# Performance work log

Hardware: AMD Instinct MI355X
Metric: run time of the kernel (lower is better)

## Reference

```python
import jax, jax.numpy as jnp
import numpy as np

B = 2048          # query batch
DIM = 256         # embedding dim (first component timelike)
SLOTS = 65536     # memory slots, count N == SLOTS (full memory)
K_TOP = 32
SIM_THRESHOLD = 0.0
LOOP_EPS = 1e-3
DECAY = 0.99


def setup_inputs() -> dict:
    key = jax.random.key(0)
    k1, k2, k3 = jax.random.split(key, 3)
    q = jax.random.normal(k1, (B, DIM), dtype=jnp.float32)
    mem = jax.random.normal(k2, (SLOTS, DIM), dtype=jnp.float32)
    age = jax.random.uniform(k3, (SLOTS,), dtype=jnp.float32) * 50.0
    return {"q": q, "mem": mem, "age": age}


def _eigen_similarity(q, mem):
    # Lorentz-invariant (Minkowski) similarity, normalized to [-1, 1].
    # metric = diag(+1, -1, ..., -1): first component timelike.
    d = q.shape[-1]
    metric = jnp.concatenate([jnp.ones((1,), q.dtype), -jnp.ones((d - 1,), q.dtype)])
    inner = jnp.einsum('bd,nd->bn', q * metric, mem)              # (B, N)
    qn = jnp.sqrt(jnp.abs(jnp.sum(q * q * metric, axis=-1))) + 1e-6   # (B,)
    mn = jnp.sqrt(jnp.abs(jnp.sum(mem * mem * metric, axis=-1))) + 1e-6  # (N,)
    return jnp.clip(inner / (qn[:, None] * mn[None, :]), -1.0, 1.0)


def reference(q, mem, age):
    sim = _eigen_similarity(q, mem)                               # (B, N)
    # loop prevention: |sim| < eps treated as self/lightlike -> zeroed
    sim = jnp.where(jnp.abs(sim) < LOOP_EPS, jnp.zeros_like(sim), sim)
    # threshold mask: disconnected entries -> -inf
    sim = jnp.where(sim <= SIM_THRESHOLD, -jnp.inf, sim)
    # temporal decay as additive log-bias
    decay_factor = jnp.clip(DECAY ** age, 1e-6, None)             # (N,)
    sim = sim + jnp.log(decay_factor)[None, :]
    sim_topk, idx_topk = jax.lax.top_k(sim, K_TOP)                # (B, k) each
    attn = jax.nn.softmax(sim_topk, axis=-1)                      # (B, k)
    mem_topk = mem[idx_topk]                                      # (B, k, D) gather
    retrieved = jnp.einsum('bk,bkd->bd', attn, mem_topk)          # (B, D)
    return retrieved
```

## Files before the change

kernel.cpp:

```cpp
#include <hip/hip_runtime.h>
#include <hip/hip_bf16.h>
#include <math.h>

#define BQ 2048
#define DIM 256
#define SLOTS 65536
#define KTOP 32
#define CAP 256
#define LCAP 10
#define POOL 48
#define TAU0 0.11f

typedef __attribute__((ext_vector_type(8))) short short8;
typedef __attribute__((ext_vector_type(4))) float f32x4;
typedef unsigned long long u64;

__device__ inline unsigned mono(float f) {
    unsigned u = __float_as_uint(f);
    return u ^ ((0u - (u >> 31)) | 0x80000000u);
}

__device__ inline ushort f2bf(float x) {
    __hip_bfloat16 h = __float2bfloat16(x);
    return *(ushort*)&h;
}

__device__ __forceinline__ void gl2lds16(const void* g, void* l) {
    __builtin_amdgcn_global_load_lds((__attribute__((address_space(1))) void*)(void*)g,
                                     (__attribute__((address_space(3))) void*)l, 16, 0, 0);
}

__global__ __launch_bounds__(256) void prep_mem_k(
    const float* __restrict__ mem, const float* __restrict__ age,
    ushort* __restrict__ mhat, float* __restrict__ mn, float* __restrict__ logdec,
    unsigned* __restrict__ counts)
{
    int t = threadIdx.x, lane = t & 63, w = t >> 6;
    if (blockIdx.x < BQ / 256) counts[blockIdx.x * 256 + t] = 0u;
    int slot = blockIdx.x * 4 + w;
    const float4* row = (const float4*)(mem + (size_t)slot * DIM);
    float4 v = row[lane];
    float p = -(v.x*v.x + v.y*v.y + v.z*v.z + v.w*v.w);
    if (lane == 0) p += 2.f * v.x * v.x;
    for (int m = 1; m < 64; m <<= 1) p += __shfl_xor(p, m);
    float nv = sqrtf(fabsf(p)) + 1e-6f;
    if (lane == 0) {
        mn[slot] = nv;
        float df = powf(0.99f, age[slot]);
        if (df < 1e-6f) df = 1e-6f;
        logdec[slot] = logf(df);
    }
    float inv = 1.f / nv;
    ushort4 o;
    o.x = f2bf(v.x * inv); o.y = f2bf(v.y * inv);
    o.z = f2bf(v.z * inv); o.w = f2bf(v.w * inv);
    *(ushort4*)&mhat[(size_t)slot * DIM + lane * 4] = o;
}

__global__ __launch_bounds__(256) void prep_q_k(
    const float* __restrict__ q, ushort* __restrict__ qhat, float* __restrict__ qs)
{
    int t = threadIdx.x, lane = t & 63, w = t >> 6;
    int b = blockIdx.x * 4 + w;
    const float4* row = (const float4*)(q + (size_t)b * DIM);
    float4 v = row[lane];
    float p = -(v.x*v.x + v.y*v.y + v.z*v.z + v.w*v.w);
    if (lane == 0) p += 2.f * v.x * v.x;
    for (int m = 1; m < 64; m <<= 1) p += __shfl_xor(p, m);
    float nv = sqrtf(fabsf(p)) + 1e-6f;
    float inv = 1.f / nv;
    float4 sv;
    sv.x = (lane == 0) ? v.x * inv : -v.x * inv;
    sv.y = -v.y * inv; sv.z = -v.z * inv; sv.w = -v.w * inv;
    *(float4*)&qs[(size_t)b * DIM + lane * 4] = sv;
    ushort4 o;
    o.x = f2bf(sv.x); o.y = f2bf(sv.y); o.z = f2bf(sv.z); o.w = f2bf(sv.w);
    *(ushort4*)&qhat[(size_t)b * DIM + lane * 4] = o;
}

__global__ __launch_bounds__(256) void screen_k(
    const ushort* __restrict__ qhat, const ushort* __restrict__ mhat,
    const float* __restrict__ logdec,
    unsigned* __restrict__ counts, u64* __restrict__ cand)
{
    __shared__ __align__(16) short At[2 * 128 * 32];
    __shared__ __align__(16) short Bt[2 * 128 * 32];
    __shared__ float tauS[128];
    __shared__ unsigned lcount[128];
    __shared__ u64 lbuf[128 * LCAP];

    int t = threadIdx.x;
    int id = blockIdx.x;
    int xcd = id & 7, slot = id >> 3;
    int rg = slot & 15, cgl = slot >> 4;
    int row0 = rg * 128;
    int col0 = (cgl * 8 + xcd) * 128;
    if (t < 128) { tauS[t] = TAU0 - logdec[col0 + t]; lcount[t] = 0u; }

    int lane = t & 63, w = t >> 6;
    int wr = (w & 1) * 64, wc = (w >> 1) * 64;
    int l15 = lane & 15, qk = (lane >> 4) * 8;
    f32x4 acc[4][4] = {};

    for (int kc = 0; kc < DIM; kc += 64) {
        __syncthreads();
        #pragma unroll
        for (int s = 0; s < 4; ++s) {
            int chunk = s * 256 + t;
            int p = chunk >> 9, rem = chunk & 511;
            int row = rem >> 2, c = rem & 3;
            char* baseA = (char*)At + s * 4096 + w * 1024;
            char* baseB = (char*)Bt + s * 4096 + w * 1024;
            gl2lds16(qhat + (size_t)(row0 + row) * DIM + kc + p * 32 + c * 8, baseA);
            gl2lds16(mhat + (size_t)(col0 + row) * DIM + kc + p * 32 + c * 8, baseB);
        }
        __syncthreads();
        #pragma unroll
        for (int p = 0; p < 2; ++p) {
            short8 af[4], bf[4];
            #pragma unroll
            for (int i = 0; i < 4; ++i)
                af[i] = *(const short8*)&At[p * 4096 + (wr + i * 16 + l15) * 32 + qk];
            #pragma unroll
            for (int i = 0; i < 4; ++i)
                bf[i] = *(const short8*)&Bt[p * 4096 + (wc + i * 16 + l15) * 32 + qk];
            #pragma unroll
            for (int i = 0; i < 4; ++i)
                #pragma unroll
                for (int j = 0; j < 4; ++j)
                    acc[i][j] = __builtin_amdgcn_mfma_f32_16x16x32_bf16(af[i], bf[j], acc[i][j], 0, 0, 0);
        }
    }

    int rquad = (lane >> 4) * 4;
    for (int i = 0; i < 4; ++i)
        for (int j = 0; j < 4; ++j) {
            int coll = wc + j * 16 + l15;
            float tau = tauS[coll];
            float ld = TAU0 - tau;
            for (int rg2 = 0; rg2 < 4; ++rg2) {
                float s = acc[i][j][rg2];
                if (s > tau) {
                    int rloc = wr + i * 16 + rquad + rg2;
                    unsigned p = atomicAdd(&lcount[rloc], 1u);
                    if (p < LCAP)
                        lbuf[rloc * LCAP + p] =
                            (((u64)mono(s + ld)) << 32) | (unsigned)(col0 + coll);
                }
            }
        }
    __syncthreads();

    if (t < 128) {
        int n = (int)lcount[t]; if (n > LCAP) n = LCAP;
        if (n > 0) {
            unsigned base = atomicAdd(&counts[row0 + t], (unsigned)n);
            for (int k = 0; k < n; ++k) {
                unsigned pos = base + (unsigned)k;
                if (pos < CAP)
                    cand[(size_t)(row0 + t) * CAP + pos] = lbuf[t * LCAP + k];
            }
        }
    }
}

__global__ __launch_bounds__(256, 4) void rescore_finalize_k(
    const float* __restrict__ qs, const float* __restrict__ mem,
    const float* __restrict__ mn, const float* __restrict__ logdec,
    const unsigned* __restrict__ counts, const u64* __restrict__ cand,
    float* __restrict__ out)
{
    __shared__ __align__(16) float qsh[DIM];
    __shared__ u64 ckey[CAP];
    __shared__ int sidx[POOL];
    __shared__ float es[POOL];
    __shared__ u64 ek[POOL];
    __shared__ float aw[KTOP];
    __shared__ int aidx[KTOP];
    __shared__ float red4a[4], red4b[4];

    int b = blockIdx.x, t = threadIdx.x;
    int lane = t & 63, wv = t >> 6;
    int cnt = (int)counts[b];
    if (cnt > CAP) cnt = CAP;
    int T = cnt < POOL ? cnt : POOL;

    qsh[t] = qs[(size_t)b * DIM + t];
    if (t < KTOP) { aw[t] = 0.f; aidx[t] = 0; }
    if (t < cnt) {
        u64 raw = cand[(size_t)b * CAP + t];
        ckey[t] = raw ^ 0xFFFFFFFFull;
    }
    __syncthreads();

    if (t < cnt) {
        u64 mykey = ckey[t];
        int rank = 0;
        for (int j = 0; j < cnt; ++j) rank += (ckey[j] > mykey);
        if (rank < POOL) sidx[rank] = (int)(~(unsigned)(mykey & 0xFFFFFFFFull));
    }
    if (t >= T && t < POOL) { es[t] = -1e30f; ek[t] = 0ull; }
    __syncthreads();

    {
        const float4* q4 = (const float4*)qsh;
        float4 qv = q4[lane];
        for (int c = wv; c < T; c += 4) {
            int si = sidx[c];
            float4 mv = ((const float4*)(mem + (size_t)si * DIM))[lane];
            float part = qv.x*mv.x + qv.y*mv.y + qv.z*mv.z + qv.w*mv.w;
            #pragma unroll
            for (int m = 1; m < 64; m <<= 1) part += __shfl_xor(part, m);
            if (lane == 0) {
                float sim = part / mn[si];
                sim = fminf(fmaxf(sim, -1.f), 1.f);
                if (fabsf(sim) < 1e-3f) sim = 0.f;
                float sc = (sim > 0.f) ? sim + logdec[si] : -1e30f;
                es[c] = sc;
                ek[c] = (((u64)mono(sc)) << 32) | (unsigned)(~(unsigned)si);
            }
        }
    }
    __syncthreads();

    float msc = -1e30f; int midx = 0; int mrank = KTOP;
    if (t < POOL) {
        u64 mykey = ek[t];
        int rank = 0;
        #pragma unroll
        for (int j = 0; j < POOL; ++j) rank += (ek[j] > mykey);
        if (rank < KTOP && es[t] > -1e29f) {
            msc = es[t];
            midx = (int)(~(unsigned)(mykey & 0xFFFFFFFFull));
            mrank = rank;
        }
    }
    float lmax = msc;
    #pragma unroll
    for (int m = 1; m < 64; m <<= 1) lmax = fmaxf(lmax, __shfl_xor(lmax, m));
    if (lane == 0) red4a[wv] = lmax;
    __syncthreads();
    float ms = fmaxf(fmaxf(red4a[0], red4a[1]), fmaxf(red4a[2], red4a[3]));

    float e = (mrank < KTOP) ? expf(msc - ms) : 0.f;
    if (mrank < KTOP) { aw[mrank] = e; aidx[mrank] = midx; }
    float ps = e;
    #pragma unroll
    for (int m = 1; m < 64; m <<= 1) ps += __shfl_xor(ps, m);
    if (lane == 0) red4b[wv] = ps;
    __syncthreads();
    float S = red4b[0] + red4b[1] + red4b[2] + red4b[3];
    float invS = (S > 0.f) ? 1.f / S : 0.f;

    float o = 0.f;
    for (int r0 = 0; r0 < KTOP; r0 += 8) {
        float w8[8]; int i8[8];
        #pragma unroll
        for (int u = 0; u < 8; ++u) { w8[u] = aw[r0 + u]; i8[u] = aidx[r0 + u]; }
        float p8[8];
        #pragma unroll
        for (int u = 0; u < 8; ++u) p8[u] = mem[(size_t)i8[u] * DIM + t];
        #pragma unroll
        for (int u = 0; u < 8; ++u) o += w8[u] * p8[u];
    }
    out[(size_t)b * DIM + t] = o * invS;
}

extern "C" void kernel_launch(void* const* d_in, const int* in_sizes, int n_in,
                              void* d_out, int out_size, void* d_ws, size_t ws_size,
                              hipStream_t stream)
{
    const float* q   = (const float*)d_in[0];
    const float* mem = (const float*)d_in[1];
    const float* age = (const float*)d_in[2];
    float* out = (float*)d_out;

    char* ws = (char*)d_ws;
    size_t off = 0;
    auto alloc = [&](size_t bytes) { size_t o = off; off = (off + bytes + 255) & ~255UL; return o; };
    ushort*   mhat   = (ushort*)(ws + alloc((size_t)SLOTS * DIM * 2));
    ushort*   qhat   = (ushort*)(ws + alloc((size_t)BQ * DIM * 2));
    float*    qs     = (float*)(ws + alloc((size_t)BQ * DIM * 4));
    float*    mn     = (float*)(ws + alloc((size_t)SLOTS * 4));
    float*    logdec = (float*)(ws + alloc((size_t)SLOTS * 4));
    unsigned* counts = (unsigned*)(ws + alloc((size_t)BQ * 4));
    u64*      cand   = (u64*)(ws + alloc((size_t)BQ * CAP * 8));

    hipLaunchKernelGGL(prep_mem_k, dim3(SLOTS / 4), dim3(256), 0, stream,
                       mem, age, mhat, mn, logdec, counts);
    hipLaunchKernelGGL(prep_q_k, dim3(BQ / 4), dim3(256), 0, stream, q, qhat, qs);
    hipLaunchKernelGGL(screen_k, dim3((BQ / 128) * (SLOTS / 128)), dim3(256), 0, stream,
                       qhat, mhat, logdec, counts, cand);
    hipLaunchKernelGGL(rescore_finalize_k, dim3(BQ), dim3(256), 0, stream,
                       qs, mem, mn, logdec, counts, cand, out);
}
```

Baseline: 230.8 us.

## Double-buffer screen GEMM with swizzled LDS and direct global candidate atomics

```diff
diff --git a/kernel.cpp b/kernel.cpp
--- a/kernel.cpp
+++ b/kernel.cpp
@@ -7,13 +7,13 @@
 #define SLOTS 65536
 #define KTOP 32
 #define CAP 256
-#define LCAP 10
 #define POOL 48
 #define TAU0 0.11f
 
 typedef __attribute__((ext_vector_type(8))) short short8;
 typedef __attribute__((ext_vector_type(4))) float f32x4;
 typedef unsigned long long u64;
+typedef __attribute__((address_space(3))) const char* lds_cp;
 
 __device__ inline unsigned mono(float f) {
     unsigned u = __float_as_uint(f);
@@ -28,6 +28,12 @@
 __device__ __forceinline__ void gl2lds16(const void* g, void* l) {
     __builtin_amdgcn_global_load_lds((__attribute__((address_space(1))) void*)(void*)g,
                                      (__attribute__((address_space(3))) void*)l, 16, 0, 0);
+}
+
+__device__ __forceinline__ short8 dsr128(lds_cp p) {
+    short8 d;
+    asm volatile("ds_read_b128 %0, %1" : "=v"(d) : "v"(p));
+    return d;
 }
 
 __global__ __launch_bounds__(256) void prep_mem_k(
@@ -78,90 +84,101 @@
     *(ushort4*)&qhat[(size_t)b * DIM + lane * 4] = o;
 }
 
-__global__ __launch_bounds__(256) void screen_k(
+__global__ __launch_bounds__(256, 3) void screen_k(
     const ushort* __restrict__ qhat, const ushort* __restrict__ mhat,
     const float* __restrict__ logdec,
     unsigned* __restrict__ counts, u64* __restrict__ cand)
 {
-    __shared__ __align__(16) short At[2 * 128 * 32];
-    __shared__ __align__(16) short Bt[2 * 128 * 32];
+    __shared__ __align__(16) short As[2][4096];
+    __shared__ __align__(16) short Bs[2][4096];
     __shared__ float tauS[128];
-    __shared__ unsigned lcount[128];
-    __shared__ u64 lbuf[128 * LCAP];
 
     int t = threadIdx.x;
     int id = blockIdx.x;
-    int xcd = id & 7, slot = id >> 3;
-    int rg = slot & 15, cgl = slot >> 4;
+    int xcd = id & 7, sid = id >> 3;
+    int rg = sid & 15, cgl = sid >> 4;
     int row0 = rg * 128;
     int col0 = (cgl * 8 + xcd) * 128;
-    if (t < 128) { tauS[t] = TAU0 - logdec[col0 + t]; lcount[t] = 0u; }
+    if (t < 128) tauS[t] = TAU0 - logdec[col0 + t];
 
     int lane = t & 63, w = t >> 6;
-    int wr = (w & 1) * 64, wc = (w >> 1) * 64;
-    int l15 = lane & 15, qk = (lane >> 4) * 8;
+    int wr = (w >> 1) * 64, wc = (w & 1) * 64;
+    int l15 = lane & 15, hi = lane >> 4;
+
+    int r0 = t >> 2, cl0 = t & 3;
+    const ushort* aS = qhat + (size_t)(row0 + r0) * DIM + (cl0 ^ ((r0 >> 1) & 3)) * 8;
+    const ushort* bS = mhat + (size_t)(col0 + r0) * DIM + (cl0 ^ ((r0 >> 1) & 3)) * 8;
+    int wb = w * 1024;
+
     f32x4 acc[4][4] = {};
-
-    for (int kc = 0; kc < DIM; kc += 64) {
-        __syncthreads();
-        #pragma unroll
-        for (int s = 0; s < 4; ++s) {
-            int chunk = s * 256 + t;
-            int p = chunk >> 9, rem = chunk & 511;
-            int row = rem >> 2, c = rem & 3;
-            char* baseA = (char*)At + s * 4096 + w * 1024;
-            char* baseB = (char*)Bt + s * 4096 + w * 1024;
-            gl2lds16(qhat + (size_t)(row0 + row) * DIM + kc + p * 32 + c * 8, baseA);
-            gl2lds16(mhat + (size_t)(col0 + row) * DIM + kc + p * 32 + c * 8, baseB);
-        }
-        __syncthreads();
-        #pragma unroll
-        for (int p = 0; p < 2; ++p) {
-            short8 af[4], bf[4];
-            #pragma unroll
-            for (int i = 0; i < 4; ++i)
-                af[i] = *(const short8*)&At[p * 4096 + (wr + i * 16 + l15) * 32 + qk];
-            #pragma unroll
-            for (int i = 0; i < 4; ++i)
-                bf[i] = *(const short8*)&Bt[p * 4096 + (wc + i * 16 + l15) * 32 + qk];
-            #pragma unroll
-            for (int i = 0; i < 4; ++i)
-                #pragma unroll
-                for (int j = 0; j < 4; ++j)
-                    acc[i][j] = __builtin_amdgcn_mfma_f32_16x16x32_bf16(af[i], bf[j], acc[i][j], 0, 0, 0);
-        }
-    }
-
-    int rquad = (lane >> 4) * 4;
+    short8 af[4], bf[4];
+
+    #define STAGE(kt) do { \
+        const int s_ = (kt) & 1; const int ke_ = (kt) * 32; \
+        gl2lds16(aS + ke_, (char*)As[s_] + wb); \
+        gl2lds16(aS + 64 * DIM + ke_, (char*)As[s_] + 4096 + wb); \
+        gl2lds16(bS + ke_, (char*)Bs[s_] + wb); \
+        gl2lds16(bS + 64 * DIM + ke_, (char*)Bs[s_] + 4096 + wb); \
+    } while (0)
+
+    int axk = (hi ^ ((l15 >> 1) & 3)) * 16;
+    lds_cp aBase = (lds_cp)(const char*)&As[0][0] + (wr + l15) * 64 + axk;
+    lds_cp bBase = (lds_cp)(const char*)&Bs[0][0] + (wc + l15) * 64 + axk;
+
+    STAGE(0); STAGE(1);
+
+    #define ITER(kt) do { \
+        if ((kt) <= 6) asm volatile("s_waitcnt vmcnt(4)" ::: "memory");   \
+        else           asm volatile("s_waitcnt vmcnt(0)" ::: "memory"); \
+        __builtin_amdgcn_s_barrier();              \
+        { lds_cp a_ = aBase + ((kt) & 1) * 8192; \
+          lds_cp b_ = bBase + ((kt) & 1) * 8192; \
+          bf[0]=dsr128(b_);      bf[1]=dsr128(b_+1024); \
+          bf[2]=dsr128(b_+2048); bf[3]=dsr128(b_+3072); \
+          af[0]=dsr128(a_);      af[1]=dsr128(a_+1024); \
+          af[2]=dsr128(a_+2048); af[3]=dsr128(a_+3072); } \
+        asm volatile("s_waitcnt lgkmcnt(0)" ::: "memory"); \
+        __builtin_amdgcn_sched_barrier(0); \
+        __builtin_amdgcn_s_barrier();              \
+        if ((kt) <= 5) STAGE((kt) + 2);            \
+        __builtin_amdgcn_sched_barrier(0); \
+        __builtin_amdgcn_s_setprio(1); \
+        _Pragma("unroll") \
+        for (int i_ = 0; i_ < 4; ++i_) { \
+            _Pragma("unroll") \
+            for (int j_ = 0; j_ < 4; ++j_) \
+                acc[i_][j_] = __builtin_amdgcn_mfma_f32_16x16x32_bf16(af[i_], bf[j_], acc[i_][j_], 0, 0, 0); \
+        } \
+        __builtin_amdgcn_s_setprio(0); \
+        __builtin_amdgcn_sched_barrier(0); \
+    } while (0)
+
+    ITER(0); ITER(1); ITER(2); ITER(3);
+    ITER(4); ITER(5); ITER(6); ITER(7);
+
+    #undef ITER
+    #undef STAGE
+
+    int rq = hi * 4;
+    #pragma unroll
     for (int i = 0; i < 4; ++i)
+        #pragma unroll
         for (int j = 0; j < 4; ++j) {
             int coll = wc + j * 16 + l15;
             float tau = tauS[coll];
             float ld = TAU0 - tau;
-            for (int rg2 = 0; rg2 < 4; ++rg2) {
-                float s = acc[i][j][rg2];
-                if (s > tau) {
-                    int rloc = wr + i * 16 + rquad + rg2;
-                    unsigned p = atomicAdd(&lcount[rloc], 1u);
-                    if (p < LCAP)
-                        lbuf[rloc * LCAP + p] =
-                            (((u64)mono(s + ld)) << 32) | (unsigned)(col0 + coll);
+            #pragma unroll
+            for (int g = 0; g < 4; ++g) {
+                float sv = acc[i][j][g];
+                if (sv > tau) {
+                    int grow = row0 + wr + i * 16 + rq + g;
+                    unsigned p = atomicAdd(&counts[grow], 1u);
+                    if (p < CAP)
+                        cand[(size_t)grow * CAP + p] =
+                            (((u64)mono(sv + ld)) << 32) | (unsigned)(col0 + coll);
                 }
             }
         }
-    __syncthreads();
-
-    if (t < 128) {
-        int n = (int)lcount[t]; if (n > LCAP) n = LCAP;
-        if (n > 0) {
-            unsigned base = atomicAdd(&counts[row0 + t], (unsigned)n);
-            for (int k = 0; k < n; ++k) {
-                unsigned pos = base + (unsigned)k;
-                if (pos < CAP)
-                    cand[(size_t)(row0 + t) * CAP + pos] = lbuf[t * LCAP + k];
-            }
-        }
-    }
 }
 
 __global__ __launch_bounds__(256, 4) void rescore_finalize_k(
```

New measurement: 241.9 us. +4.8%, slower.

## Restructure screen GEMM as persistent blocks with LDS-resident queries; fuse prep kernels

Applied to the files above, without the earlier changes.

```diff
diff --git a/kernel.cpp b/kernel.cpp
--- a/kernel.cpp
+++ b/kernel.cpp
@@ -7,7 +7,6 @@
 #define SLOTS 65536
 #define KTOP 32
 #define CAP 256
-#define LCAP 10
 #define POOL 48
 #define TAU0 0.11f
 
@@ -30,141 +29,131 @@
                                      (__attribute__((address_space(3))) void*)l, 16, 0, 0);
 }
 
-__global__ __launch_bounds__(256) void prep_mem_k(
+__global__ __launch_bounds__(256) void prep_k(
     const float* __restrict__ mem, const float* __restrict__ age,
+    const float* __restrict__ q,
     ushort* __restrict__ mhat, float* __restrict__ mn, float* __restrict__ logdec,
+    ushort* __restrict__ qhat, float* __restrict__ qs,
     unsigned* __restrict__ counts)
 {
     int t = threadIdx.x, lane = t & 63, w = t >> 6;
     if (blockIdx.x < BQ / 256) counts[blockIdx.x * 256 + t] = 0u;
     int slot = blockIdx.x * 4 + w;
-    const float4* row = (const float4*)(mem + (size_t)slot * DIM);
-    float4 v = row[lane];
-    float p = -(v.x*v.x + v.y*v.y + v.z*v.z + v.w*v.w);
-    if (lane == 0) p += 2.f * v.x * v.x;
-    for (int m = 1; m < 64; m <<= 1) p += __shfl_xor(p, m);
-    float nv = sqrtf(fabsf(p)) + 1e-6f;
-    if (lane == 0) {
-        mn[slot] = nv;
-        float df = powf(0.99f, age[slot]);
-        if (df < 1e-6f) df = 1e-6f;
-        logdec[slot] = logf(df);
-    }
-    float inv = 1.f / nv;
-    ushort4 o;
-    o.x = f2bf(v.x * inv); o.y = f2bf(v.y * inv);
-    o.z = f2bf(v.z * inv); o.w = f2bf(v.w * inv);
-    *(ushort4*)&mhat[(size_t)slot * DIM + lane * 4] = o;
-}
-
-__global__ __launch_bounds__(256) void prep_q_k(
-    const float* __restrict__ q, ushort* __restrict__ qhat, float* __restrict__ qs)
-{
-    int t = threadIdx.x, lane = t & 63, w = t >> 6;
-    int b = blockIdx.x * 4 + w;
-    const float4* row = (const float4*)(q + (size_t)b * DIM);
-    float4 v = row[lane];
-    float p = -(v.x*v.x + v.y*v.y + v.z*v.z + v.w*v.w);
-    if (lane == 0) p += 2.f * v.x * v.x;
-    for (int m = 1; m < 64; m <<= 1) p += __shfl_xor(p, m);
-    float nv = sqrtf(fabsf(p)) + 1e-6f;
-    float inv = 1.f / nv;
-    float4 sv;
-    sv.x = (lane == 0) ? v.x * inv : -v.x * inv;
-    sv.y = -v.y * inv; sv.z = -v.z * inv; sv.w = -v.w * inv;
-    *(float4*)&qs[(size_t)b * DIM + lane * 4] = sv;
-    ushort4 o;
-    o.x = f2bf(sv.x); o.y = f2bf(sv.y); o.z = f2bf(sv.z); o.w = f2bf(sv.w);
-    *(ushort4*)&qhat[(size_t)b * DIM + lane * 4] = o;
-}
-
-__global__ __launch_bounds__(256) void screen_k(
+    {
+        const float4* row = (const float4*)(mem + (size_t)slot * DIM);
+        float4 v = row[lane];
+        float p = -(v.x*v.x + v.y*v.y + v.z*v.z + v.w*v.w);
+        if (lane == 0) p += 2.f * v.x * v.x;
+        for (int m = 1; m < 64; m <<= 1) p += __shfl_xor(p, m);
+        float nv = sqrtf(fabsf(p)) + 1e-6f;
+        if (lane == 0) {
+            mn[slot] = nv;
+            float ldv = age[slot] * -0.010050335853501441f;
+            if (ldv < -13.815510557964274f) ldv = -13.815510557964274f;
+            logdec[slot] = ldv;
+        }
+        float inv = 1.f / nv;
+        ushort4 o;
+        o.x = f2bf(v.x * inv); o.y = f2bf(v.y * inv);
+        o.z = f2bf(v.z * inv); o.w = f2bf(v.w * inv);
+        *(ushort4*)&mhat[(size_t)slot * DIM + lane * 4] = o;
+    }
+    if (blockIdx.x < BQ / 4) {
+        int b = blockIdx.x * 4 + w;
+        const float4* row = (const float4*)(q + (size_t)b * DIM);
+        float4 v = row[lane];
+        float p = -(v.x*v.x + v.y*v.y + v.z*v.z + v.w*v.w);
+        if (lane == 0) p += 2.f * v.x * v.x;
+        for (int m = 1; m < 64; m <<= 1) p += __shfl_xor(p, m);
+        float nv = sqrtf(fabsf(p)) + 1e-6f;
+        float inv = 1.f / nv;
+        float4 sv;
+        sv.x = (lane == 0) ? v.x * inv : -v.x * inv;
+        sv.y = -v.y * inv; sv.z = -v.z * inv; sv.w = -v.w * inv;
+        *(float4*)&qs[(size_t)b * DIM + lane * 4] = sv;
+        ushort4 o;
+        o.x = f2bf(sv.x); o.y = f2bf(sv.y); o.z = f2bf(sv.z); o.w = f2bf(sv.w);
+        *(ushort4*)&qhat[(size_t)b * DIM + lane * 4] = o;
+    }
+}
+
+__global__ __launch_bounds__(256, 2) void screen_k(
     const ushort* __restrict__ qhat, const ushort* __restrict__ mhat,
     const float* __restrict__ logdec,
     unsigned* __restrict__ counts, u64* __restrict__ cand)
 {
-    __shared__ __align__(16) short At[2 * 128 * 32];
-    __shared__ __align__(16) short Bt[2 * 128 * 32];
-    __shared__ float tauS[128];
-    __shared__ unsigned lcount[128];
-    __shared__ u64 lbuf[128 * LCAP];
-
-    int t = threadIdx.x;
+    __shared__ __align__(16) short Al[8][128][32];
+
+    int t = threadIdx.x, lane = t & 63, w = t >> 6;
     int id = blockIdx.x;
-    int xcd = id & 7, slot = id >> 3;
-    int rg = slot & 15, cgl = slot >> 4;
+    int xcd = id & 7, lid = id >> 3;
+    int rg = lid & 15, sw = lid >> 4;
     int row0 = rg * 128;
-    int col0 = (cgl * 8 + xcd) * 128;
-    if (t < 128) { tauS[t] = TAU0 - logdec[col0 + t]; lcount[t] = 0u; }
-
-    int lane = t & 63, w = t >> 6;
-    int wr = (w & 1) * 64, wc = (w >> 1) * 64;
-    int l15 = lane & 15, qk = (lane >> 4) * 8;
-    f32x4 acc[4][4] = {};
-
-    for (int kc = 0; kc < DIM; kc += 64) {
-        __syncthreads();
-        #pragma unroll
-        for (int s = 0; s < 4; ++s) {
-            int chunk = s * 256 + t;
-            int p = chunk >> 9, rem = chunk & 511;
-            int row = rem >> 2, c = rem & 3;
-            char* baseA = (char*)At + s * 4096 + w * 1024;
-            char* baseB = (char*)Bt + s * 4096 + w * 1024;
-            gl2lds16(qhat + (size_t)(row0 + row) * DIM + kc + p * 32 + c * 8, baseA);
-            gl2lds16(mhat + (size_t)(col0 + row) * DIM + kc + p * 32 + c * 8, baseB);
-        }
-        __syncthreads();
-        #pragma unroll
-        for (int p = 0; p < 2; ++p) {
-            short8 af[4], bf[4];
+    int colbase = (xcd * 4 + sw) * 2048;
+
+    #pragma unroll
+    for (int s = 0; s < 16; ++s) {
+        int c = s * 256 + t;
+        int kt = c >> 9, row = (c >> 2) & 127, sl = c & 3;
+        int lsl = sl ^ ((row >> 1) & 3);
+        gl2lds16(qhat + (size_t)(row0 + row) * DIM + kt * 32 + lsl * 8,
+                 (char*)Al + (s * 256 + w * 64) * 16);
+    }
+    asm volatile("s_waitcnt vmcnt(0)" ::: "memory");
+    __syncthreads();
+
+    int l15 = lane & 15, hi = lane >> 4;
+    int wm = w >> 1, wn = w & 1;
+    int aslot = (hi ^ ((l15 >> 1) & 3)) * 8;
+
+    const ushort* bp0 = mhat + (size_t)(colbase + wn * 1024 +  0 + l15) * DIM + hi * 8;
+    const ushort* bp1 = mhat + (size_t)(colbase + wn * 1024 + 16 + l15) * DIM + hi * 8;
+    const ushort* bp2 = mhat + (size_t)(colbase + wn * 1024 + 32 + l15) * DIM + hi * 8;
+    const ushort* bp3 = mhat + (size_t)(colbase + wn * 1024 + 48 + l15) * DIM + hi * 8;
+
+    for (int ct = 0; ct < 16; ++ct) {
+        f32x4 acc[4][4] = {};
+        size_t cto = (size_t)ct * 64 * DIM;
+        #pragma unroll
+        for (int kt = 0; kt < 8; ++kt) {
+            short8 bf[4], af[4];
+            bf[0] = *(const short8*)(bp0 + cto + kt * 32);
+            bf[1] = *(const short8*)(bp1 + cto + kt * 32);
+            bf[2] = *(const short8*)(bp2 + cto + kt * 32);
+            bf[3] = *(const short8*)(bp3 + cto + kt * 32);
             #pragma unroll
             for (int i = 0; i < 4; ++i)
-                af[i] = *(const short8*)&At[p * 4096 + (wr + i * 16 + l15) * 32 + qk];
-            #pragma unroll
-            for (int i = 0; i < 4; ++i)
-                bf[i] = *(const short8*)&Bt[p * 4096 + (wc + i * 16 + l15) * 32 + qk];
+                af[i] = *(const short8*)&Al[kt][wm * 64 + i * 16 + l15][aslot];
             #pragma unroll
             for (int i = 0; i < 4; ++i)
                 #pragma unroll
                 for (int j = 0; j < 4; ++j)
                     acc[i][j] = __builtin_amdgcn_mfma_f32_16x16x32_bf16(af[i], bf[j], acc[i][j], 0, 0, 0);
         }
-    }
-
-    int rquad = (lane >> 4) * 4;
-    for (int i = 0; i < 4; ++i)
+        int colt = colbase + wn * 1024 + ct * 64;
+        #pragma unroll
         for (int j = 0; j < 4; ++j) {
-            int coll = wc + j * 16 + l15;
-            float tau = tauS[coll];
-            float ld = TAU0 - tau;
-            for (int rg2 = 0; rg2 < 4; ++rg2) {
-                float s = acc[i][j][rg2];
-                if (s > tau) {
-                    int rloc = wr + i * 16 + rquad + rg2;
-                    unsigned p = atomicAdd(&lcount[rloc], 1u);
-                    if (p < LCAP)
-                        lbuf[rloc * LCAP + p] =
-                            (((u64)mono(s + ld)) << 32) | (unsigned)(col0 + coll);
+            int coll = colt + j * 16 + l15;
+            float ld = logdec[coll];
+            float tau = TAU0 - ld;
+            #pragma unroll
+            for (int i = 0; i < 4; ++i)
+                #pragma unroll
+                for (int g = 0; g < 4; ++g) {
+                    float sv = acc[i][j][g];
+                    if (sv > tau) {
+                        int grow = row0 + wm * 64 + i * 16 + hi * 4 + g;
+                        unsigned p = atomicAdd(&counts[grow], 1u);
+                        if (p < CAP)
+                            cand[(size_t)grow * CAP + p] =
+                                (((u64)mono(sv + ld)) << 32) | (unsigned)coll;
+                    }
                 }
-            }
-        }
-    __syncthreads();
-
-    if (t < 128) {
-        int n = (int)lcount[t]; if (n > LCAP) n = LCAP;
-        if (n > 0) {
-            unsigned base = atomicAdd(&counts[row0 + t], (unsigned)n);
-            for (int k = 0; k < n; ++k) {
-                unsigned pos = base + (unsigned)k;
-                if (pos < CAP)
-                    cand[(size_t)(row0 + t) * CAP + pos] = lbuf[t * LCAP + k];
-            }
-        }
-    }
-}
-
-__global__ __launch_bounds__(256, 4) void rescore_finalize_k(
+        }
+    }
+}
+
+__global__ __launch_bounds__(256, 8) void rescore_finalize_k(
     const float* __restrict__ qs, const float* __restrict__ mem,
     const float* __restrict__ mn, const float* __restrict__ logdec,
     const unsigned* __restrict__ counts, const u64* __restrict__ cand,
@@ -286,10 +275,9 @@
     unsigned* counts = (unsigned*)(ws + alloc((size_t)BQ * 4));
     u64*      cand   = (u64*)(ws + alloc((size_t)BQ * CAP * 8));
 
-    hipLaunchKernelGGL(prep_mem_k, dim3(SLOTS / 4), dim3(256), 0, stream,
-                       mem, age, mhat, mn, logdec, counts);
-    hipLaunchKernelGGL(prep_q_k, dim3(BQ / 4), dim3(256), 0, stream, q, qhat, qs);
-    hipLaunchKernelGGL(screen_k, dim3((BQ / 128) * (SLOTS / 128)), dim3(256), 0, stream,
+    hipLaunchKernelGGL(prep_k, dim3(SLOTS / 4), dim3(256), 0, stream,
+                       mem, age, q, mhat, mn, logdec, qhat, qs, counts);
+    hipLaunchKernelGGL(screen_k, dim3(512), dim3(256), 0, stream,
                        qhat, mhat, logdec, counts, cand);
     hipLaunchKernelGGL(rescore_finalize_k, dim3(BQ), dim3(256), 0, stream,
                        qs, mem, mn, logdec, counts, cand, out);
```

Result: slower. 298.0 us (+29.1%).
